# Performance work log

Measured on AMD Instinct MI355X. Metric: run time of the kernel, lower is better.

The kernel has to match this reference:

```python
import jax, jax.numpy as jnp
import numpy as np
import math

TOPK = 13
NUM_CLASSES = 80
ALPHA = 1.0
BETA = 6.0
EPS = 1e-9


def ciou_xyxy(box1, box2, eps=1e-7):
    """CIoU between xyxy boxes; box1/box2 broadcastable [..., 4]. Returns [..., 1]."""
    b1x1, b1y1, b1x2, b1y2 = jnp.split(box1, 4, axis=-1)
    b2x1, b2y1, b2x2, b2y2 = jnp.split(box2, 4, axis=-1)
    w1, h1 = b1x2 - b1x1, b1y2 - b1y1 + eps
    w2, h2 = b2x2 - b2x1, b2y2 - b2y1 + eps
    inter = (jnp.minimum(b1x2, b2x2) - jnp.maximum(b1x1, b2x1)).clip(0) * \
            (jnp.minimum(b1y2, b2y2) - jnp.maximum(b1y1, b2y1)).clip(0)
    union = w1 * h1 + w2 * h2 - inter + eps
    iou = inter / union
    cw = jnp.maximum(b1x2, b2x2) - jnp.minimum(b1x1, b2x1)
    ch = jnp.maximum(b1y2, b2y2) - jnp.minimum(b1y1, b2y1)
    c2 = cw ** 2 + ch ** 2 + eps
    rho2 = ((b2x1 + b2x2 - b1x1 - b1x2) ** 2 + (b2y1 + b2y2 - b1y1 - b1y2) ** 2) / 4
    v = (4.0 / math.pi ** 2) * (jnp.arctan(w2 / h2) - jnp.arctan(w1 / h1)) ** 2
    alpha = jax.lax.stop_gradient(v / (v - iou + (1 + eps)))  # torch.no_grad block
    return iou - (rho2 / c2 + v * alpha)


def setup_inputs() -> dict:
    key = jax.random.key(0)
    ks = jax.random.split(key, 8)
    bs, M = 16, 64
    # YOLOv8 anchor grid: strides 8/16/32 on a 640x640 image -> 8400 points
    pts = []
    for s, n in ((8, 80), (16, 40), (32, 20)):
        xs = (np.arange(n, dtype=np.float32) + 0.5) * s
        gx, gy = np.meshgrid(xs, xs)
        pts.append(np.stack([gx.ravel(), gy.ravel()], -1))
    anc_points = jnp.asarray(np.concatenate(pts, 0), jnp.float32)  # (8400, 2)
    A = anc_points.shape[0]
    pd_scores = jax.random.uniform(ks[0], (bs, A, NUM_CLASSES), jnp.float32)
    c = jax.random.uniform(ks[1], (bs, A, 2), jnp.float32) * 640.0
    wh = jax.random.uniform(ks[2], (bs, A, 2), jnp.float32) * 120.0 + 8.0
    pd_bboxes = jnp.concatenate([c - wh / 2, c + wh / 2], -1)  # xyxy
    gc = jax.random.uniform(ks[3], (bs, M, 2), jnp.float32) * 560.0 + 40.0
    gwh = jax.random.uniform(ks[4], (bs, M, 2), jnp.float32) * 200.0 + 20.0
    gt_bboxes = jnp.concatenate([gc - gwh / 2, gc + gwh / 2], -1)
    gt_labels = jax.random.randint(ks[5], (bs, M, 1), 0, NUM_CLASSES, dtype=jnp.int32)
    mask_gt = (jax.random.uniform(ks[6], (bs, M, 1)) > 0.25).astype(jnp.float32)
    return {"pd_scores": pd_scores, "pd_bboxes": pd_bboxes, "anc_points": anc_points,
            "gt_labels": gt_labels, "gt_bboxes": gt_bboxes, "mask_gt": mask_gt}


def _assign(pd_scores, pd_bboxes, anc_points, gt_labels, gt_bboxes, mask_gt):
    bs, A, nc = pd_scores.shape
    M = gt_bboxes.shape[1]
    dt = pd_scores.dtype

    # ---- select_candidates_in_gts: anchors inside gt boxes -> (b, M, A) ----
    lt = gt_bboxes[:, :, None, :2]            # (b, M, 1, 2)
    rb = gt_bboxes[:, :, None, 2:]
    xy = anc_points[None, None]               # (1, 1, A, 2)
    deltas = jnp.concatenate([xy - lt, rb - xy], axis=-1)  # (b, M, A, 4)
    mask_in_gts = (deltas.min(-1) > EPS).astype(dt)        # (b, M, A)

    # ---- get_box_metrics ----
    bidx = jnp.arange(bs)[:, None]                         # (b, 1)
    labels = gt_labels[..., 0].astype(jnp.int32)           # (b, M)
    bbox_scores = pd_scores[bidx, :, labels]               # (b, M, A)
    overlaps = ciou_xyxy(gt_bboxes[:, :, None, :], pd_bboxes[:, None, :, :])
    overlaps = overlaps[..., 0].clip(0)                    # (b, M, A)
    align_metric = bbox_scores ** ALPHA * overlaps ** BETA

    # ---- select_topk_candidates (scatter-add instead of one_hot over 8400) ----
    metrics = align_metric * mask_in_gts
    _, topk_idxs = jax.lax.top_k(metrics, TOPK)            # (b, M, topk)
    valid = mask_gt > 0                                    # (b, M, 1) bool
    topk_idxs = jnp.where(valid, topk_idxs, 0)
    counts = jnp.zeros((bs, M, A), dt).at[
        jnp.arange(bs)[:, None, None], jnp.arange(M)[None, :, None], topk_idxs
    ].add(1.0)
    mask_topk = jnp.where(counts > 1, jnp.zeros((), dt), counts)
    mask_pos = mask_topk * mask_in_gts * mask_gt           # (b, M, A)

    # ---- select_highest_overlaps (unconditional; identity when no conflicts) ----
    fg_mask = mask_pos.sum(-2)                             # (b, A)
    mask_multi = fg_mask[:, None, :] > 1                   # (b, 1, A)
    max_idx = overlaps.argmax(1)                           # (b, A)
    is_max = jnp.swapaxes(jax.nn.one_hot(max_idx, M, dtype=dt), 1, 2)  # (b, M, A)
    mask_pos = jnp.where(mask_multi, is_max, mask_pos)
    fg_mask = mask_pos.sum(-2)
    target_gt_idx = mask_pos.argmax(-2)                    # (b, A)

    # ---- get_targets ----
    flat_idx = target_gt_idx + bidx * M                    # (b, A) into b*M
    target_labels = jnp.clip(gt_labels.reshape(-1)[flat_idx], 0)   # (b, A)
    target_bboxes = gt_bboxes.reshape(-1, 4)[flat_idx]             # (b, A, 4)
    target_scores = jax.nn.one_hot(target_labels, NUM_CLASSES, dtype=dt)
    target_scores = jnp.where(fg_mask[..., None] > 0, target_scores, jnp.zeros((), dt))

    # ---- normalize scores by aligned metric ----
    align_metric = align_metric * mask_pos
    pos_align = align_metric.max(-1, keepdims=True)        # (b, M, 1)
    pos_overlaps = (overlaps * mask_pos).max(-1, keepdims=True)
    norm = (align_metric * pos_overlaps / (pos_align + EPS)).max(-2)[..., None]  # (b, A, 1)
    target_scores = target_scores * norm

    return target_labels, target_bboxes, target_scores, fg_mask.astype(bool), target_gt_idx


def reference(pd_scores, pd_bboxes, anc_points, gt_labels, gt_bboxes, mask_gt):
    return _assign(pd_scores, pd_bboxes, anc_points, gt_labels, gt_bboxes, mask_gt)
```

## Files before the change

kernel.cpp:

```cpp
#include <hip/hip_runtime.h>

#define A_TOT 8400
#define NCLS  80
#define MGT   64
#define TK    13
#define EPS7  1e-7f
#define EPS9  1e-9f
#define INV_PI2 0.4052847345693511f
#define BTH   1024
#define NIT   ((A_TOT + BTH - 1) / BTH)

__device__ __forceinline__ float ciou_clip(
    float gx1, float gy1, float gx2, float gy2, float ga, float area1,
    float px1, float py1, float px2, float py2, float pa)
{
  float w2 = px2 - px1, h2 = py2 - py1 + EPS7;
  float iw = fmaxf(fminf(gx2, px2) - fmaxf(gx1, px1), 0.f);
  float ih = fmaxf(fminf(gy2, py2) - fmaxf(gy1, py1), 0.f);
  float inter = iw * ih;
  float uni = area1 + w2 * h2 - inter + EPS7;
  float iou = inter / uni;
  float cw = fmaxf(gx2, px2) - fminf(gx1, px1);
  float ch = fmaxf(gy2, py2) - fminf(gy1, py1);
  float c2 = cw * cw + ch * ch + EPS7;
  float dx = px1 + px2 - gx1 - gx2;
  float dy = py1 + py2 - gy1 - gy2;
  float rho2 = (dx * dx + dy * dy) * 0.25f;
  float dd = pa - ga;
  float v = INV_PI2 * dd * dd;
  float alpha = v / (v - iou + (1.f + EPS7));
  float c = iou - (rho2 / c2 + v * alpha);
  return fmaxf(c, 0.f);
}

__device__ __forceinline__ unsigned long long wmax64(unsigned long long k) {
#pragma unroll
  for (int s = 32; s > 0; s >>= 1) {
    unsigned long long o = __shfl_xor(k, s, 64);
    k = (o > k) ? o : k;
  }
  return k;
}

__global__ __launch_bounds__(256)
void k_topkA(const float* __restrict__ pd_scores,
             const float* __restrict__ pd_bboxes,
             const float* __restrict__ anc,
             const int* __restrict__ gt_labels,
             const float* __restrict__ gt_bboxes,
             const float* __restrict__ mask_gt,
             int* __restrict__ topk_idx)
{
  int row = blockIdx.x;
  int tid = threadIdx.x, lane = tid & 63, wid = tid >> 6;
  __shared__ unsigned long long sk[4 * TK];

  if (mask_gt[row] <= 0.f) {
    if (tid < TK) topk_idx[row * TK + tid] = -1;
    return;
  }
  int b = row >> 6;

  float4 g = ((const float4*)gt_bboxes)[row];
  float ga = atanf((g.z - g.x) / (g.w - g.y + EPS7));
  float area1 = (g.z - g.x) * (g.w - g.y + EPS7);
  int label = gt_labels[row];
  const float*  ps   = pd_scores + (size_t)b * A_TOT * NCLS + label;
  const float4* pb   = (const float4*)(pd_bboxes + (size_t)b * A_TOT * 4);
  const float2* anc2 = (const float2*)anc;

  unsigned long long l[TK];
#pragma unroll
  for (int k = 0; k < TK; ++k) l[k] = 0ULL;

  auto insert = [&](unsigned long long key) {
    if (key > l[TK - 1]) {
#pragma unroll
      for (int j = TK - 1; j > 0; --j) {
        unsigned long long prev = l[j - 1];
        l[j] = (key > prev) ? prev : ((key > l[j]) ? key : l[j]);
      }
      l[0] = (key > l[0]) ? key : l[0];
    }
  };
  auto eval_inbox = [&](int a) -> unsigned long long {
    float4 p = pb[a];
    float pa = atanf((p.z - p.x) / (p.w - p.y + EPS7));
    float ov = ciou_clip(g.x, g.y, g.z, g.w, ga, area1, p.x, p.y, p.z, p.w, pa);
    float o2 = ov * ov;
    float metric = ps[(size_t)a * NCLS] * (o2 * o2 * o2);
    return (((unsigned long long)__float_as_uint(metric)) << 32) |
           (unsigned long long)(~(unsigned)a);
  };

  {
    int a = tid;
    float2 an = anc2[a];
    float dmin = fminf(fminf(an.x - g.x, an.y - g.y), fminf(g.z - an.x, g.w - an.y));
    unsigned long long key = (unsigned long long)(~(unsigned)a);
    if (dmin > EPS9) key = eval_inbox(a);
    insert(key);
  }

  const int   ns[3] = {80, 40, 20};
  const float ss[3] = {8.f, 16.f, 32.f};
  const int   bb[3] = {0, 6400, 8000};
#pragma unroll
  for (int sc = 0; sc < 3; ++sc) {
    int n = ns[sc]; float s = ss[sc]; int base = bb[sc];
    float inv_s = 1.f / s;
    int xlo = max(0,     (int)floorf(g.x * inv_s - 0.5f));
    int xhi = min(n - 1, (int)ceilf (g.z * inv_s - 0.5f));
    int ylo = max(0,     (int)floorf(g.y * inv_s - 0.5f));
    int yhi = min(n - 1, (int)ceilf (g.w * inv_s - 0.5f));
    int nx = xhi - xlo + 1, ny = yhi - ylo + 1;
    if (nx <= 0 || ny <= 0) continue;
    int tot = nx * ny;
    float invnx = 1.f / (float)nx;
    for (int r = tid; r < tot; r += 256) {
      int q  = (int)floorf(((float)r + 0.5f) * invnx);
      int ix = xlo + (r - q * nx);
      int iy = ylo + q;
      int a = base + iy * n + ix;
      if (a < 256) continue;
      float ax = ((float)ix + 0.5f) * s;
      float ay = ((float)iy + 0.5f) * s;
      float dmin = fminf(fminf(ax - g.x, ay - g.y), fminf(g.z - ax, g.w - ay));
      if (dmin > EPS9) insert(eval_inbox(a));
    }
  }

  unsigned long long wres = 0ULL;
#pragma unroll
  for (int r = 0; r < TK; ++r) {
    unsigned long long w = wmax64(l[0]);
    if (lane == r) wres = w;
    if (l[0] == w) {
#pragma unroll
      for (int j = 0; j < TK - 1; ++j) l[j] = l[j + 1];
      l[TK - 1] = 0ULL;
    }
  }
  if (lane < TK) sk[wid * TK + lane] = wres;
  __syncthreads();

  if (wid == 0) {
    unsigned long long c = (lane < 4 * TK) ? sk[lane] : 0ULL;
    unsigned long long res = 0ULL;
#pragma unroll
    for (int r = 0; r < TK; ++r) {
      unsigned long long w = wmax64(c);
      if (lane == r) res = w;
      if (c == w) c = 0ULL;
    }
    if (lane < TK) {
      unsigned a = ~(unsigned)res;
      float2 an = anc2[a];
      float dmin = fminf(fminf(an.x - g.x, an.y - g.y), fminf(g.z - an.x, g.w - an.y));
      topk_idx[row * TK + lane] = (dmin > EPS9) ? (int)a : -1;
    }
  }
}

__global__ __launch_bounds__(BTH)
void k_resolveB(const float* __restrict__ pd_scores,
                const float* __restrict__ pd_bboxes,
                const int* __restrict__ gt_labels,
                const float* __restrict__ gt_bboxes,
                const int* __restrict__ topk_idx,
                unsigned long long* __restrict__ pk)
{
  int b = blockIdx.x;
  int tid = threadIdx.x, lane = tid & 63;
  __shared__ unsigned int cntm[A_TOT];
  __shared__ float4 sg[MGT];
  __shared__ float  sga[MGT], sarea[MGT];
  __shared__ int    slabm[MGT];
  __shared__ unsigned int spal[MGT], spov[MGT];

  for (int i = tid; i < A_TOT; i += BTH) cntm[i] = 0u;
  if (tid < MGT) {
    float4 g = ((const float4*)gt_bboxes)[b * MGT + tid];
    sg[tid] = g;
    sga[tid] = atanf((g.z - g.x) / (g.w - g.y + EPS7));
    sarea[tid] = (g.z - g.x) * (g.w - g.y + EPS7);
    slabm[tid] = gt_labels[b * MGT + tid];
    spal[tid] = 0u; spov[tid] = 0u;
  }
  __syncthreads();

  if (tid < MGT * TK) {
    int a = topk_idx[b * MGT * TK + tid];
    if (a >= 0) atomicAdd(&cntm[a], (1u << 16) | (unsigned)(tid / TK));
  }
  __syncthreads();

  const float4* pb = (const float4*)pd_bboxes + (size_t)b * A_TOT;
  const float*  ps = pd_scores + (size_t)b * A_TOT * NCLS;

  int   rtgt[NIT];
  float ram[NIT];

#pragma unroll
  for (int it = 0; it < NIT; ++it) {
    int a = tid + it * BTH;
    bool valid = a < A_TOT;
    unsigned cm = valid ? cntm[a] : 0u;
    int cnt = (int)(cm >> 16);
    float4 p = make_float4(0.f, 0.f, 0.f, 0.f);
    float pa = 0.f;
    if (valid && cnt > 0) {
      p = pb[a];
      pa = atanf((p.z - p.x) / (p.w - p.y + EPS7));
    }
    int mytgt = -1; float myam = 0.f;
    if (valid && cnt == 1) {
      int m = (int)(cm & 0xffffu);
      float4 g = sg[m];
      float ov = ciou_clip(g.x, g.y, g.z, g.w, sga[m], sarea[m],
                           p.x, p.y, p.z, p.w, pa);
      float o2 = ov * ov;
      myam = ps[(size_t)a * NCLS + slabm[m]] * (o2 * o2 * o2);
      mytgt = m;
      atomicMax(&spal[m], __float_as_uint(myam));
      atomicMax(&spov[m], __float_as_uint(ov));
    }
    unsigned long long mb = __ballot(valid && cnt > 1);
    while (mb) {
      int src = __ffsll(mb) - 1; mb &= mb - 1;
      int   aa  = __shfl(a, src);
      float px1 = __shfl(p.x, src), py1 = __shfl(p.y, src);
      float px2 = __shfl(p.z, src), py2 = __shfl(p.w, src);
      float spa = __shfl(pa, src);
      float4 g = sg[lane];
      float ov = ciou_clip(g.x, g.y, g.z, g.w, sga[lane], sarea[lane],
                           px1, py1, px2, py2, spa);
      unsigned long long key =
          (((unsigned long long)__float_as_uint(ov)) << 6) | (unsigned)(63 - lane);
      unsigned long long w = wmax64(key);
      int   wl  = 63 - (int)(w & 63ULL);
      float wov = __uint_as_float((unsigned)(w >> 6));
      float am_s = 0.f;
      if (lane == wl) {
        float o2 = wov * wov;
        am_s = ps[(size_t)aa * NCLS + slabm[wl]] * (o2 * o2 * o2);
        atomicMax(&spal[wl], __float_as_uint(am_s));
        atomicMax(&spov[wl], __float_as_uint(wov));
      }
      am_s = __shfl(am_s, wl);
      if (lane == src) { mytgt = wl; myam = am_s; }
    }
    rtgt[it] = mytgt; ram[it] = myam;
  }
  __syncthreads();

#pragma unroll
  for (int it = 0; it < NIT; ++it) {
    int a = tid + it * BTH;
    if (a >= A_TOT) continue;
    int mytgt = rtgt[it];
    bool fg = mytgt >= 0;
    int tgt = fg ? mytgt : 0;
    int lab = slabm[tgt]; if (lab < 0) lab = 0;
    float nrm = 0.f;
    if (fg) {
      float pal = __uint_as_float(spal[tgt]);
      float pov = __uint_as_float(spov[tgt]);
      nrm = ram[it] * pov / (pal + EPS9);
    }
    unsigned lo = (unsigned)tgt | ((unsigned)lab << 8) | ((fg ? 1u : 0u) << 24);
    pk[(size_t)b * A_TOT + a] =
        (((unsigned long long)__float_as_uint(nrm)) << 32) | lo;
  }
}

__global__ __launch_bounds__(256)
void k_writeC(const unsigned long long* __restrict__ pk,
              const float* __restrict__ gt_bboxes,
              float* __restrict__ out, int total)
{
  __shared__ int   slab[256];
  __shared__ float snorm[256];
  int base = blockIdx.x * 256, tid = threadIdx.x;
  int t = base + tid;
  int nrows = total - base; if (nrows > 256) nrows = 256;
  size_t OFF_BOX = (size_t)total;
  size_t OFF_SCR = OFF_BOX + (size_t)total * 4;
  size_t OFF_FG  = OFF_SCR + (size_t)total * NCLS;
  size_t OFF_TGT = OFF_FG + (size_t)total;
  int lab = 0; float nrm = 0.f;
  if (t < total) {
    unsigned long long v = pk[t];
    unsigned lo = (unsigned)v;
    int tgt = (int)(lo & 0xffu);
    lab = (int)((lo >> 8) & 0xffu);
    bool fg = (lo >> 24) & 1u;
    nrm = __uint_as_float((unsigned)(v >> 32));
    int b = t / A_TOT;
    float4 box = ((const float4*)gt_bboxes)[b * MGT + tgt];
    out[t] = (float)lab;
    ((float4*)(out + OFF_BOX))[t] = box;
    out[OFF_FG + t]  = fg ? 1.f : 0.f;
    out[OFF_TGT + t] = (float)tgt;
  }
  slab[tid]  = lab;
  snorm[tid] = nrm;
  __syncthreads();
  float4* srow = (float4*)(out + OFF_SCR + (size_t)base * NCLS);
  int nvec = nrows * (NCLS / 4);
  for (int u = tid; u < nvec; u += 256) {
    int i  = u / (NCLS / 4);
    int c0 = (u - i * (NCLS / 4)) * 4;
    int lb = slab[i]; float nv = snorm[i];
    float4 v;
    v.x = (lb == c0    ) ? nv : 0.f;
    v.y = (lb == c0 + 1) ? nv : 0.f;
    v.z = (lb == c0 + 2) ? nv : 0.f;
    v.w = (lb == c0 + 3) ? nv : 0.f;
    srow[u] = v;
  }
}

extern "C" void kernel_launch(void* const* d_in, const int* in_sizes, int n_in,
                              void* d_out, int out_size, void* d_ws, size_t ws_size,
                              hipStream_t stream)
{
  const float* pd_scores = (const float*)d_in[0];
  const float* pd_bboxes = (const float*)d_in[1];
  const float* anc       = (const float*)d_in[2];
  const int*   gt_labels = (const int*)d_in[3];
  const float* gt_bboxes = (const float*)d_in[4];
  const float* mask_gt   = (const float*)d_in[5];
  int bs = in_sizes[0] / (A_TOT * NCLS);
  int NA = bs * A_TOT, NM = bs * MGT;

  unsigned long long* pk = (unsigned long long*)d_ws;
  int* topk_idx = (int*)(pk + NA);

  k_topkA<<<NM, 256, 0, stream>>>(pd_scores, pd_bboxes, anc, gt_labels,
                                  gt_bboxes, mask_gt, topk_idx);
  k_resolveB<<<bs, BTH, 0, stream>>>(pd_scores, pd_bboxes, gt_labels,
                                     gt_bboxes, topk_idx, pk);
  k_writeC<<<(NA + 255) / 256, 256, 0, stream>>>(pk, gt_bboxes,
                                                 (float*)d_out, NA);
}
```

Measured before the change: 137.4 us.

## Split resolve kernel across anchor windows with global atomic per-GT maxima

The resolve stage ran one 1024-thread block per image, 16 blocks in total, and looped over all 8400 anchors. It now launches one block per 1024-anchor window per image, which gives many more blocks to occupy the GPU. Because each block sees only part of the anchors, the per-GT max align and overlap values move from shared memory into global arrays, updated with global atomicMax. These arrays are zeroed by the top-k kernel, and the normalisation step moves into the write kernel. The cost is extra global atomics, extra global reads in the final kernel, and each block redundantly reading all top-k indices.

```diff
diff --git a/kernel.cpp b/kernel.cpp
--- a/kernel.cpp
+++ b/kernel.cpp
@@ -8,7 +8,7 @@
 #define EPS9  1e-9f
 #define INV_PI2 0.4052847345693511f
 #define BTH   1024
-#define NIT   ((A_TOT + BTH - 1) / BTH)
+#define NWIN  ((A_TOT + BTH - 1) / BTH)
 
 __device__ __forceinline__ float ciou_clip(
     float gx1, float gy1, float gx2, float gy2, float ga, float area1,
@@ -49,11 +49,15 @@
              const int* __restrict__ gt_labels,
              const float* __restrict__ gt_bboxes,
              const float* __restrict__ mask_gt,
-             int* __restrict__ topk_idx)
+             int* __restrict__ topk_idx,
+             unsigned int* __restrict__ pos_al,
+             unsigned int* __restrict__ pos_ov)
 {
   int row = blockIdx.x;
   int tid = threadIdx.x, lane = tid & 63, wid = tid >> 6;
   __shared__ unsigned long long sk[4 * TK];
+
+  if (tid == 0) { pos_al[row] = 0u; pos_ov[row] = 0u; }
 
   if (mask_gt[row] <= 0.f) {
     if (tid < TK) topk_idx[row * TK + tid] = -1;
@@ -168,114 +172,103 @@
                 const int* __restrict__ gt_labels,
                 const float* __restrict__ gt_bboxes,
                 const int* __restrict__ topk_idx,
+                unsigned int* __restrict__ pos_al,
+                unsigned int* __restrict__ pos_ov,
                 unsigned long long* __restrict__ pk)
 {
-  int b = blockIdx.x;
+  int b = blockIdx.x / NWIN;
+  int s = blockIdx.x - b * NWIN;
+  int lo = s * BTH;
   int tid = threadIdx.x, lane = tid & 63;
-  __shared__ unsigned int cntm[A_TOT];
+
+  __shared__ unsigned int cntm[BTH];
   __shared__ float4 sg[MGT];
   __shared__ float  sga[MGT], sarea[MGT];
   __shared__ int    slabm[MGT];
-  __shared__ unsigned int spal[MGT], spov[MGT];
-
-  for (int i = tid; i < A_TOT; i += BTH) cntm[i] = 0u;
+
+  cntm[tid] = 0u;
   if (tid < MGT) {
     float4 g = ((const float4*)gt_bboxes)[b * MGT + tid];
     sg[tid] = g;
     sga[tid] = atanf((g.z - g.x) / (g.w - g.y + EPS7));
     sarea[tid] = (g.z - g.x) * (g.w - g.y + EPS7);
     slabm[tid] = gt_labels[b * MGT + tid];
-    spal[tid] = 0u; spov[tid] = 0u;
   }
   __syncthreads();
 
   if (tid < MGT * TK) {
     int a = topk_idx[b * MGT * TK + tid];
-    if (a >= 0) atomicAdd(&cntm[a], (1u << 16) | (unsigned)(tid / TK));
+    int r = a - lo;
+    if (a >= 0 && r >= 0 && r < BTH)
+      atomicAdd(&cntm[r], (1u << 16) | (unsigned)(tid / TK));
   }
   __syncthreads();
 
   const float4* pb = (const float4*)pd_bboxes + (size_t)b * A_TOT;
   const float*  ps = pd_scores + (size_t)b * A_TOT * NCLS;
 
-  int   rtgt[NIT];
-  float ram[NIT];
-
-#pragma unroll
-  for (int it = 0; it < NIT; ++it) {
-    int a = tid + it * BTH;
-    bool valid = a < A_TOT;
-    unsigned cm = valid ? cntm[a] : 0u;
-    int cnt = (int)(cm >> 16);
-    float4 p = make_float4(0.f, 0.f, 0.f, 0.f);
-    float pa = 0.f;
-    if (valid && cnt > 0) {
-      p = pb[a];
-      pa = atanf((p.z - p.x) / (p.w - p.y + EPS7));
-    }
-    int mytgt = -1; float myam = 0.f;
-    if (valid && cnt == 1) {
-      int m = (int)(cm & 0xffffu);
-      float4 g = sg[m];
-      float ov = ciou_clip(g.x, g.y, g.z, g.w, sga[m], sarea[m],
-                           p.x, p.y, p.z, p.w, pa);
-      float o2 = ov * ov;
-      myam = ps[(size_t)a * NCLS + slabm[m]] * (o2 * o2 * o2);
-      mytgt = m;
-      atomicMax(&spal[m], __float_as_uint(myam));
-      atomicMax(&spov[m], __float_as_uint(ov));
-    }
-    unsigned long long mb = __ballot(valid && cnt > 1);
-    while (mb) {
-      int src = __ffsll(mb) - 1; mb &= mb - 1;
-      int   aa  = __shfl(a, src);
-      float px1 = __shfl(p.x, src), py1 = __shfl(p.y, src);
-      float px2 = __shfl(p.z, src), py2 = __shfl(p.w, src);
-      float spa = __shfl(pa, src);
-      float4 g = sg[lane];
-      float ov = ciou_clip(g.x, g.y, g.z, g.w, sga[lane], sarea[lane],
-                           px1, py1, px2, py2, spa);
-      unsigned long long key =
-          (((unsigned long long)__float_as_uint(ov)) << 6) | (unsigned)(63 - lane);
-      unsigned long long w = wmax64(key);
-      int   wl  = 63 - (int)(w & 63ULL);
-      float wov = __uint_as_float((unsigned)(w >> 6));
-      float am_s = 0.f;
-      if (lane == wl) {
-        float o2 = wov * wov;
-        am_s = ps[(size_t)aa * NCLS + slabm[wl]] * (o2 * o2 * o2);
-        atomicMax(&spal[wl], __float_as_uint(am_s));
-        atomicMax(&spov[wl], __float_as_uint(wov));
-      }
-      am_s = __shfl(am_s, wl);
-      if (lane == src) { mytgt = wl; myam = am_s; }
-    }
-    rtgt[it] = mytgt; ram[it] = myam;
-  }
-  __syncthreads();
-
-#pragma unroll
-  for (int it = 0; it < NIT; ++it) {
-    int a = tid + it * BTH;
-    if (a >= A_TOT) continue;
-    int mytgt = rtgt[it];
+  int a = lo + tid;
+  bool valid = a < A_TOT;
+  unsigned cm = valid ? cntm[tid] : 0u;
+  int cnt = (int)(cm >> 16);
+  float4 p = make_float4(0.f, 0.f, 0.f, 0.f);
+  float pa = 0.f;
+  if (valid && cnt > 0) {
+    p = pb[a];
+    pa = atanf((p.z - p.x) / (p.w - p.y + EPS7));
+  }
+  int mytgt = -1; float myam = 0.f;
+  if (valid && cnt == 1) {
+    int m = (int)(cm & 0xffffu);
+    float4 g = sg[m];
+    float ov = ciou_clip(g.x, g.y, g.z, g.w, sga[m], sarea[m],
+                         p.x, p.y, p.z, p.w, pa);
+    float o2 = ov * ov;
+    myam = ps[(size_t)a * NCLS + slabm[m]] * (o2 * o2 * o2);
+    mytgt = m;
+    atomicMax(pos_al + b * MGT + m, __float_as_uint(myam));
+    atomicMax(pos_ov + b * MGT + m, __float_as_uint(ov));
+  }
+  unsigned long long mb = __ballot(valid && cnt > 1);
+  while (mb) {
+    int src = __ffsll(mb) - 1; mb &= mb - 1;
+    int   aa  = __shfl(a, src);
+    float px1 = __shfl(p.x, src), py1 = __shfl(p.y, src);
+    float px2 = __shfl(p.z, src), py2 = __shfl(p.w, src);
+    float spa = __shfl(pa, src);
+    float4 g = sg[lane];
+    float ov = ciou_clip(g.x, g.y, g.z, g.w, sga[lane], sarea[lane],
+                         px1, py1, px2, py2, spa);
+    unsigned long long key =
+        (((unsigned long long)__float_as_uint(ov)) << 6) | (unsigned)(63 - lane);
+    unsigned long long w = wmax64(key);
+    int   wl  = 63 - (int)(w & 63ULL);
+    float wov = __uint_as_float((unsigned)(w >> 6));
+    float am_s = 0.f;
+    if (lane == wl) {
+      float o2 = wov * wov;
+      am_s = ps[(size_t)aa * NCLS + slabm[wl]] * (o2 * o2 * o2);
+      atomicMax(pos_al + b * MGT + wl, __float_as_uint(am_s));
+      atomicMax(pos_ov + b * MGT + wl, __float_as_uint(wov));
+    }
+    am_s = __shfl(am_s, wl);
+    if (lane == src) { mytgt = wl; myam = am_s; }
+  }
+
+  if (valid) {
     bool fg = mytgt >= 0;
     int tgt = fg ? mytgt : 0;
     int lab = slabm[tgt]; if (lab < 0) lab = 0;
-    float nrm = 0.f;
-    if (fg) {
-      float pal = __uint_as_float(spal[tgt]);
-      float pov = __uint_as_float(spov[tgt]);
-      nrm = ram[it] * pov / (pal + EPS9);
-    }
-    unsigned lo = (unsigned)tgt | ((unsigned)lab << 8) | ((fg ? 1u : 0u) << 24);
+    unsigned lov = (unsigned)tgt | ((unsigned)lab << 8) | ((fg ? 1u : 0u) << 24);
     pk[(size_t)b * A_TOT + a] =
-        (((unsigned long long)__float_as_uint(nrm)) << 32) | lo;
+        (((unsigned long long)__float_as_uint(myam)) << 32) | lov;
   }
 }
 
 __global__ __launch_bounds__(256)
 void k_writeC(const unsigned long long* __restrict__ pk,
+              const unsigned int* __restrict__ pos_al,
+              const unsigned int* __restrict__ pos_ov,
               const float* __restrict__ gt_bboxes,
               float* __restrict__ out, int total)
 {
@@ -291,13 +284,19 @@
   int lab = 0; float nrm = 0.f;
   if (t < total) {
     unsigned long long v = pk[t];
-    unsigned lo = (unsigned)v;
-    int tgt = (int)(lo & 0xffu);
-    lab = (int)((lo >> 8) & 0xffu);
-    bool fg = (lo >> 24) & 1u;
-    nrm = __uint_as_float((unsigned)(v >> 32));
+    unsigned lov = (unsigned)v;
+    int tgt = (int)(lov & 0xffu);
+    lab = (int)((lov >> 8) & 0xffu);
+    bool fg = (lov >> 24) & 1u;
     int b = t / A_TOT;
-    float4 box = ((const float4*)gt_bboxes)[b * MGT + tgt];
+    int gi = b * MGT + tgt;
+    if (fg) {
+      float am  = __uint_as_float((unsigned)(v >> 32));
+      float pal = __uint_as_float(pos_al[gi]);
+      float pov = __uint_as_float(pos_ov[gi]);
+      nrm = am * pov / (pal + EPS9);
+    }
+    float4 box = ((const float4*)gt_bboxes)[gi];
     out[t] = (float)lab;
     ((float4*)(out + OFF_BOX))[t] = box;
     out[OFF_FG + t]  = fg ? 1.f : 0.f;
@@ -336,11 +335,14 @@
 
   unsigned long long* pk = (unsigned long long*)d_ws;
   int* topk_idx = (int*)(pk + NA);
+  unsigned int* pos_al = (unsigned int*)(topk_idx + NM * TK);
+  unsigned int* pos_ov = pos_al + NM;
 
   k_topkA<<<NM, 256, 0, stream>>>(pd_scores, pd_bboxes, anc, gt_labels,
-                                  gt_bboxes, mask_gt, topk_idx);
-  k_resolveB<<<bs, BTH, 0, stream>>>(pd_scores, pd_bboxes, gt_labels,
-                                     gt_bboxes, topk_idx, pk);
-  k_writeC<<<(NA + 255) / 256, 256, 0, stream>>>(pk, gt_bboxes,
+                                  gt_bboxes, mask_gt, topk_idx, pos_al, pos_ov);
+  k_resolveB<<<bs * NWIN, BTH, 0, stream>>>(pd_scores, pd_bboxes, gt_labels,
+                                            gt_bboxes, topk_idx, pos_al,
+                                            pos_ov, pk);
+  k_writeC<<<(NA + 255) / 256, 256, 0, stream>>>(pk, pos_al, pos_ov, gt_bboxes,
                                                  (float*)d_out, NA);
 }
```

After: 124.6 us. -9.3%, faster.
